# Kernel optimization log

Hardware: AMD Instinct MI355X
Metric: run time of the kernel (lower is better)

The kernel has to match this reference:

```python
import jax, jax.numpy as jnp
import numpy as np

BH, BW = 64, 64            # base model input (block) size
STRIDE = 16                # block // 4, per WindowObjectDetector.predict
N_CLASSES = 10
THRESH = 0.7


def _extract_patches(x, bh, bw, stride):
    # x: [1, H, W, 3] -> [R, C, bh, bw, 3], VALID padding (tf.image.extract_patches)
    H, W = x.shape[1], x.shape[2]
    R = (H - bh) // stride + 1
    C = (W - bw) // stride + 1
    r = (jnp.arange(R) * stride)[:, None] + jnp.arange(bh)   # [R, bh]
    c = (jnp.arange(C) * stride)[:, None] + jnp.arange(bw)   # [C, bw]
    p = x[0][r]                 # [R, bh, W, 3]
    p = p[:, :, c]              # [R, bh, C, bw, 3]
    return jnp.transpose(p, (0, 2, 1, 3, 4))  # [R, C, bh, bw, 3]


def _connected_components(mask):
    # mask: bool [K, R, C]; 4-connectivity min-label propagation.
    K, R, C = mask.shape
    BIG = jnp.int32(R * C + 2)
    seed = (jnp.arange(R * C, dtype=jnp.int32).reshape(R, C) + 1)[None]  # [1,R,C]
    lbl0 = jnp.where(mask, seed, 0)

    def prop(l):
        xm = jnp.where(mask, l, BIG)
        n = xm
        n = jnp.minimum(n, jnp.pad(xm, ((0, 0), (1, 0), (0, 0)), constant_values=R * C + 2)[:, :R, :])
        n = jnp.minimum(n, jnp.pad(xm, ((0, 0), (0, 1), (0, 0)), constant_values=R * C + 2)[:, 1:, :])
        n = jnp.minimum(n, jnp.pad(xm, ((0, 0), (0, 0), (1, 0)), constant_values=R * C + 2)[:, :, :C])
        n = jnp.minimum(n, jnp.pad(xm, ((0, 0), (0, 0), (0, 1)), constant_values=R * C + 2)[:, :, 1:])
        return jnp.where(mask, n, 0)

    def cond(carry):
        prev, cur = carry
        return jnp.any(prev != cur)

    def body(carry):
        _, cur = carry
        return cur, prop(cur)

    _, lbl = jax.lax.while_loop(cond, body, (lbl0, prop(lbl0)))
    return lbl  # [K, R, C] int32, 0 = background


def _boxes_from_labels(labels):
    # labels: [K, R, C] -> padded boxes [K, R*C+1, 4] (rowmin-1, colmin-1, rowmax+1, colmax+1)
    K, R, C = labels.shape
    S = R * C + 1
    rr = jnp.repeat(jnp.arange(R, dtype=jnp.int32), C)  # [R*C]
    cc = jnp.tile(jnp.arange(C, dtype=jnp.int32), R)
    flat = labels.reshape(K, R * C)

    def per_class(lbl_k):
        rmin = jax.ops.segment_min(rr, lbl_k, num_segments=S)
        rmax = jax.ops.segment_max(rr, lbl_k, num_segments=S)
        cmin = jax.ops.segment_min(cc, lbl_k, num_segments=S)
        cmax = jax.ops.segment_max(cc, lbl_k, num_segments=S)
        cnt = jax.ops.segment_sum(jnp.ones_like(lbl_k), lbl_k, num_segments=S)
        valid = (cnt > 0) & (jnp.arange(S) > 0)
        box = jnp.stack([rmin - 1, cmin - 1, rmax + 1, cmax + 1], axis=-1)
        box = jnp.where(valid[:, None], box, -1)
        return box, valid

    return jax.vmap(per_class)(flat)


def setup_inputs() -> dict:
    key = jax.random.key(0)
    k1, k2, k3 = jax.random.split(key, 3)
    inputs = jax.random.uniform(k1, (1, 1024, 1024, 3), dtype=jnp.float32)
    W = jax.random.normal(k2, (BH * BW * 3, N_CLASSES), dtype=jnp.float32) * 0.02
    b = jax.random.normal(k3, (N_CLASSES,), dtype=jnp.float32)
    return {"inputs": inputs, "W": W, "b": b}


def reference(inputs, W, b):
    # Windowing: extract 64x64 patches with stride 16 (image divisible by 64 -> no resize)
    patches = _extract_patches(inputs, BH, BW, STRIDE)          # [R, C, 64, 64, 3]
    R, C = patches.shape[0], patches.shape[1]
    flat = patches.reshape(R * C, BH * BW * 3)
    logits = flat @ W + b                                        # base model
    prob = jax.nn.softmax(logits, axis=1).reshape(R, C, N_CLASSES)
    mask = prob > THRESH                                         # [R, C, K]
    # tf transposes before/after connected_components (4-connectivity is symmetric)
    labels = _connected_components(jnp.transpose(mask, (2, 0, 1)))  # [K, R, C]
    labels = jnp.transpose(labels, (1, 2, 0))                    # [R, C, K]
    boxes, valid = _boxes_from_labels(jnp.transpose(labels, (2, 0, 1)))
    return prob, labels, boxes, valid
```

## Files before the change

### kernel.cpp

```cpp
#include <hip/hip_runtime.h>
#include <math.h>

#define RG 61
#define CG 61
#define NP 3721
#define NSEG 3722
#define NCLS 10
#define KTOT 12288
#define NPATCH 8
#define THRESHV 0.7f
#define BIGI 0x3FFFFFFF

__global__ __launch_bounds__(256) void wod_logits(
    const float* __restrict__ img,
    const float* __restrict__ W,
    const float* __restrict__ bias,
    float* __restrict__ out_prob,
    int* __restrict__ mask)
{
    const int tid = threadIdx.x;
    const int blk = blockIdx.x;
    const int r   = blk >> 3;
    const int c0  = (blk & 7) * NPATCH;
    const int np  = (CG - c0) < NPATCH ? (CG - c0) : NPATCH;

    float acc[NPATCH][NCLS];
    #pragma unroll
    for (int p = 0; p < NPATCH; ++p)
        #pragma unroll
        for (int k = 0; k < NCLS; ++k) acc[p][k] = 0.f;

    const float* imgr = img + (16 * r) * 3072 + c0 * 48;

    for (int pi = tid; pi < KTOT / 2; pi += 256) {
        const int e   = pi << 1;
        const int i   = e / 192;
        const int rem = e - i * 192;
        const float* wp = W + e * NCLS;
        const float4 wa = *(const float4*)(wp);
        const float4 wb = *(const float4*)(wp + 4);
        const float4 wc = *(const float4*)(wp + 8);
        const float4 wd = *(const float4*)(wp + 12);
        const float4 we = *(const float4*)(wp + 16);
        const float w0[NCLS] = {wa.x, wa.y, wa.z, wa.w, wb.x, wb.y, wb.z, wb.w, wc.x, wc.y};
        const float w1[NCLS] = {wc.z, wc.w, wd.x, wd.y, wd.z, wd.w, we.x, we.y, we.z, we.w};
        const float* xb = imgr + i * 3072 + rem;
        #pragma unroll
        for (int p = 0; p < NPATCH; ++p) {
            const int po = (p < np ? p : 0) * 48;
            const float2 x = *(const float2*)(xb + po);
            #pragma unroll
            for (int k = 0; k < NCLS; ++k) {
                acc[p][k] = fmaf(x.x, w0[k], acc[p][k]);
                acc[p][k] = fmaf(x.y, w1[k], acc[p][k]);
            }
        }
    }

    #pragma unroll
    for (int p = 0; p < NPATCH; ++p)
        #pragma unroll
        for (int k = 0; k < NCLS; ++k) {
            float v = acc[p][k];
            for (int off = 32; off; off >>= 1) v += __shfl_down(v, off);
            acc[p][k] = v;
        }

    __shared__ float red[4][NPATCH][NCLS];
    __shared__ float logit[NPATCH][NCLS];
    const int wave = tid >> 6, lane = tid & 63;
    if (lane == 0)
        for (int p = 0; p < NPATCH; ++p)
            for (int k = 0; k < NCLS; ++k) red[wave][p][k] = acc[p][k];
    __syncthreads();
    if (tid < NPATCH * NCLS) {
        const int p = tid / NCLS, k = tid - p * NCLS;
        logit[p][k] = red[0][p][k] + red[1][p][k] + red[2][p][k] + red[3][p][k]
                      + bias[k];
    }
    __syncthreads();
    if (tid < np) {
        const int p = tid, c = c0 + p;
        float m = -1e30f;
        for (int k = 0; k < NCLS; ++k) m = fmaxf(m, logit[p][k]);
        float ex[NCLS], s = 0.f;
        for (int k = 0; k < NCLS; ++k) { ex[k] = expf(logit[p][k] - m); s += ex[k]; }
        const float inv = 1.f / s;
        const int cell = r * CG + c;
        const int base = cell * NCLS;
        for (int k = 0; k < NCLS; ++k) {
            const float pr = ex[k] * inv;
            out_prob[base + k] = pr;
            mask[k * NP + cell] = (pr > THRESHV) ? 1 : 0;
        }
    }
}

__global__ __launch_bounds__(256) void wod_cc(
    const int* __restrict__ mask,
    float* __restrict__ out_lbl,
    float* __restrict__ out_box,
    float* __restrict__ out_valid)
{
    const int k = blockIdx.x;
    const int tid = threadIdx.x;
    __shared__ int lbl[NP];
    __shared__ int ext0[NSEG], ext1[NSEG];
    __shared__ int changed;

    const int* mk = mask + k * NP;
    for (int idx = tid; idx < NP; idx += 256)
        lbl[idx] = mk[idx] ? (idx + 1) : 0;
    if (tid == 0) changed = 0;
    __syncthreads();

    for (;;) {
        for (int idx = tid; idx < NP; idx += 256) {
            int v = lbl[idx];
            if (v) {
                const int rr = idx / CG;
                const int cc = idx - rr * CG;
                int best = v;
                if (rr > 0)      { int n = lbl[idx - CG]; if (n && n < best) best = n; }
                if (rr < RG - 1) { int n = lbl[idx + CG]; if (n && n < best) best = n; }
                if (cc > 0)      { int n = lbl[idx - 1];  if (n && n < best) best = n; }
                if (cc < CG - 1) { int n = lbl[idx + 1];  if (n && n < best) best = n; }
                if (best < v) { lbl[idx] = best; changed = 1; }
            }
        }
        __syncthreads();
        const bool stop = (changed == 0);
        __syncthreads();
        if (stop) break;
        if (tid == 0) changed = 0;
        __syncthreads();
    }

    for (int idx = tid; idx < NP; idx += 256)
        out_lbl[idx * NCLS + k] = (float)lbl[idx];

    float* boxk = out_box + k * NSEG * 4;
    float* valk = out_valid + k * NSEG;

    for (int s = tid; s < NSEG; s += 256) { ext0[s] = BIGI; ext1[s] = BIGI; }
    __syncthreads();
    for (int idx = tid; idx < NP; idx += 256) {
        const int v = lbl[idx];
        if (v) {
            const int rr = idx / CG, cc = idx - rr * CG;
            atomicMin(&ext0[v], rr);
            atomicMin(&ext1[v], cc);
        }
    }
    __syncthreads();
    for (int s = tid; s < NSEG; s += 256) {
        const bool valid = (s > 0) && (ext0[s] != BIGI);
        boxk[s * 4 + 0] = valid ? (float)(ext0[s] - 1) : -1.f;
        boxk[s * 4 + 1] = valid ? (float)(ext1[s] - 1) : -1.f;
        valk[s] = valid ? 1.f : 0.f;
    }
    __syncthreads();

    for (int s = tid; s < NSEG; s += 256) { ext0[s] = -1; ext1[s] = -1; }
    __syncthreads();
    for (int idx = tid; idx < NP; idx += 256) {
        const int v = lbl[idx];
        if (v) {
            const int rr = idx / CG, cc = idx - rr * CG;
            atomicMax(&ext0[v], rr);
            atomicMax(&ext1[v], cc);
        }
    }
    __syncthreads();
    for (int s = tid; s < NSEG; s += 256) {
        const bool valid = (s > 0) && (ext0[s] >= 0);
        boxk[s * 4 + 2] = valid ? (float)(ext0[s] + 1) : -1.f;
        boxk[s * 4 + 3] = valid ? (float)(ext1[s] + 1) : -1.f;
    }
}

extern "C" void kernel_launch(void* const* d_in, const int* in_sizes, int n_in,
                              void* d_out, int out_size, void* d_ws, size_t ws_size,
                              hipStream_t stream) {
    (void)in_sizes; (void)n_in; (void)out_size; (void)ws_size;
    const float* img = (const float*)d_in[0];
    const float* W   = (const float*)d_in[1];
    const float* b   = (const float*)d_in[2];

    float* out       = (float*)d_out;
    float* out_prob  = out;
    float* out_lbl   = out + 37210;
    float* out_box   = out + 74420;
    float* out_valid = out + 223300;

    int* mask = (int*)d_ws;

    hipLaunchKernelGGL(wod_logits, dim3(RG * 8), dim3(256), 0, stream,
                       img, W, b, out_prob, mask);
    hipLaunchKernelGGL(wod_cc, dim3(NCLS), dim3(256), 0, stream,
                       mask, out_lbl, out_box, out_valid);
}
```

Measured before the change: 51.11 us.

## Split logits reduction dimension across blocks with separate softmax reduce kernel

The K=12288 reduction of each patch group is split into four slices handled by separate blocks, which raises the grid from 488 to 1952 blocks and gives the GPU more parallelism. The partial sums go to workspace, and a new small kernel adds them with the bias and applies softmax and the threshold mask. Inside each block the wave shuffle reduction is cut to three steps, followed by a 32-row shared-memory sum. This adds one kernel launch and a round trip of partial sums through global memory.

```diff
diff --git a/kernel.cpp b/kernel.cpp
--- a/kernel.cpp
+++ b/kernel.cpp
@@ -8,20 +8,24 @@
 #define NCLS 10
 #define KTOT 12288
 #define NPATCH 8
+#define KS 4
+#define PAIRS_SLICE 1536
+#define ITERS 6
 #define THRESHV 0.7f
 #define BIGI 0x3FFFFFFF
 
-__global__ __launch_bounds__(256) void wod_logits(
+__global__ __launch_bounds__(256) void wod_logits_part(
     const float* __restrict__ img,
     const float* __restrict__ W,
-    const float* __restrict__ bias,
-    float* __restrict__ out_prob,
-    int* __restrict__ mask)
+    float* __restrict__ part)
 {
     const int tid = threadIdx.x;
     const int blk = blockIdx.x;
-    const int r   = blk >> 3;
-    const int c0  = (blk & 7) * NPATCH;
+    const int ks  = blk & (KS - 1);
+    const int g   = blk >> 2;
+    const int r   = g >> 3;
+    const int cg  = g & 7;
+    const int c0  = cg * NPATCH;
     const int np  = (CG - c0) < NPATCH ? (CG - c0) : NPATCH;
 
     float acc[NPATCH][NCLS];
@@ -32,7 +36,9 @@
 
     const float* imgr = img + (16 * r) * 3072 + c0 * 48;
 
-    for (int pi = tid; pi < KTOT / 2; pi += 256) {
+    #pragma unroll
+    for (int it = 0; it < ITERS; ++it) {
+        const int pi  = ks * PAIRS_SLICE + it * 256 + tid;
         const int e   = pi << 1;
         const int i   = e / 192;
         const int rem = e - i * 192;
@@ -62,37 +68,67 @@
         #pragma unroll
         for (int k = 0; k < NCLS; ++k) {
             float v = acc[p][k];
-            for (int off = 32; off; off >>= 1) v += __shfl_down(v, off);
+            v += __shfl_down(v, 1);
+            v += __shfl_down(v, 2);
+            v += __shfl_down(v, 4);
             acc[p][k] = v;
         }
 
-    __shared__ float red[4][NPATCH][NCLS];
-    __shared__ float logit[NPATCH][NCLS];
-    const int wave = tid >> 6, lane = tid & 63;
-    if (lane == 0)
+    __shared__ float red[32][81];
+    const int lane = tid & 63, wave = tid >> 6;
+    if ((lane & 7) == 0) {
+        const int row = wave * 8 + (lane >> 3);
+        #pragma unroll
         for (int p = 0; p < NPATCH; ++p)
-            for (int k = 0; k < NCLS; ++k) red[wave][p][k] = acc[p][k];
+            #pragma unroll
+            for (int k = 0; k < NCLS; ++k)
+                red[row][p * NCLS + k] = acc[p][k];
+    }
     __syncthreads();
     if (tid < NPATCH * NCLS) {
-        const int p = tid / NCLS, k = tid - p * NCLS;
-        logit[p][k] = red[0][p][k] + red[1][p][k] + red[2][p][k] + red[3][p][k]
-                      + bias[k];
-    }
-    __syncthreads();
-    if (tid < np) {
-        const int p = tid, c = c0 + p;
-        float m = -1e30f;
-        for (int k = 0; k < NCLS; ++k) m = fmaxf(m, logit[p][k]);
-        float ex[NCLS], s = 0.f;
-        for (int k = 0; k < NCLS; ++k) { ex[k] = expf(logit[p][k] - m); s += ex[k]; }
-        const float inv = 1.f / s;
-        const int cell = r * CG + c;
-        const int base = cell * NCLS;
-        for (int k = 0; k < NCLS; ++k) {
-            const float pr = ex[k] * inv;
-            out_prob[base + k] = pr;
-            mask[k * NP + cell] = (pr > THRESHV) ? 1 : 0;
-        }
+        float s = 0.f;
+        #pragma unroll
+        for (int j = 0; j < 32; ++j) s += red[j][tid];
+        part[blk * (NPATCH * NCLS) + tid] = s;
+    }
+}
+
+__global__ __launch_bounds__(256) void wod_reduce(
+    const float* __restrict__ part,
+    const float* __restrict__ bias,
+    float* __restrict__ out_prob,
+    int* __restrict__ mask)
+{
+    const int cell = blockIdx.x * 256 + threadIdx.x;
+    if (cell >= NP) return;
+    const int r  = cell / CG;
+    const int c  = cell - r * CG;
+    const int cg = c >> 3;
+    const int p  = c & 7;
+    const int gb = ((r * 8 + cg) * KS) * (NPATCH * NCLS) + p * NCLS;
+
+    float lg[NCLS];
+    #pragma unroll
+    for (int k = 0; k < NCLS; ++k) lg[k] = bias[k];
+    #pragma unroll
+    for (int ks = 0; ks < KS; ++ks)
+        #pragma unroll
+        for (int k = 0; k < NCLS; ++k)
+            lg[k] += part[gb + ks * (NPATCH * NCLS) + k];
+
+    float m = -1e30f;
+    #pragma unroll
+    for (int k = 0; k < NCLS; ++k) m = fmaxf(m, lg[k]);
+    float ex[NCLS], s = 0.f;
+    #pragma unroll
+    for (int k = 0; k < NCLS; ++k) { ex[k] = expf(lg[k] - m); s += ex[k]; }
+    const float inv = 1.f / s;
+    const int base = cell * NCLS;
+    #pragma unroll
+    for (int k = 0; k < NCLS; ++k) {
+        const float pr = ex[k] * inv;
+        out_prob[base + k] = pr;
+        mask[k * NP + cell] = (pr > THRESHV) ? 1 : 0;
     }
 }
 
@@ -193,10 +229,13 @@
     float* out_box   = out + 74420;
     float* out_valid = out + 223300;
 
-    int* mask = (int*)d_ws;
-
-    hipLaunchKernelGGL(wod_logits, dim3(RG * 8), dim3(256), 0, stream,
-                       img, W, b, out_prob, mask);
+    int*   mask = (int*)d_ws;
+    float* part = (float*)d_ws + NCLS * NP;
+
+    hipLaunchKernelGGL(wod_logits_part, dim3(RG * 8 * KS), dim3(256), 0, stream,
+                       img, W, part);
+    hipLaunchKernelGGL(wod_reduce, dim3((NP + 255) / 256), dim3(256), 0, stream,
+                       part, b, out_prob, mask);
     hipLaunchKernelGGL(wod_cc, dim3(NCLS), dim3(256), 0, stream,
                        mask, out_lbl, out_box, out_valid);
 }
```

Result: slower. 59.44 us (+16.3%).
